# Kernel tuning notes

Hardware: AMD Instinct MI355X
Metric: run time of the kernel (lower is better)

## Reference

```python
import jax, jax.numpy as jnp
import numpy as np

DIM = 192
RC = 16
M = 64
LN_EPS = 1e-5
NORM_EPS = 1e-12


def _layernorm(x, g, b):
    mu = jnp.mean(x, axis=-1, keepdims=True)
    var = jnp.mean((x - mu) ** 2, axis=-1, keepdims=True)
    return (x - mu) / jnp.sqrt(var + LN_EPS) * g + b


def _l2norm(x):
    n = jnp.sqrt(jnp.sum(x * x, axis=-1, keepdims=True))
    return x / jnp.maximum(n, NORM_EPS)


def setup_inputs() -> dict:
    key = jax.random.key(0)
    ks = jax.random.split(key, 12)
    B, N = 8, 16384
    s_q = 1.0 / np.sqrt(DIM)
    inp = {
        "x": jax.random.normal(ks[0], (B, N, DIM), jnp.float32),
        "dict_tokens": jax.random.normal(ks[1], (B, M, DIM), jnp.float32),
        "H": 128,
        "W": 128,
        "wq_w": jax.random.normal(ks[2], (DIM, RC), jnp.float32) * s_q,
        "wq_b": jnp.zeros((RC,), jnp.float32),
        "wk_w": jax.random.normal(ks[3], (DIM, RC), jnp.float32) * s_q,
        "wk_b": jnp.zeros((RC,), jnp.float32),
        "wv_w": jax.random.normal(ks[4], (DIM, DIM), jnp.float32) * s_q,
        "wv_b": jnp.zeros((DIM,), jnp.float32),
        "qn_g": jnp.ones((RC,), jnp.float32),
        "qn_b": jnp.zeros((RC,), jnp.float32),
        "kn_g": jnp.ones((RC,), jnp.float32),
        "kn_b": jnp.zeros((RC,), jnp.float32),
        "conv_w": jax.random.normal(ks[5], (DIM, 1, 3, 3), jnp.float32) / 3.0,
        "conv_b": jnp.zeros((DIM,), jnp.float32),
        "temperature": jnp.ones((1,), jnp.float32),
    }
    return inp


def reference(x, dict_tokens, H, W, wq_w, wq_b, wk_w, wk_b, wv_w, wv_b,
              qn_g, qn_b, kn_g, kn_b, conv_w, conv_b, temperature):
    # q: (B,N,rc), k: (B,M,rc)
    q = _l2norm(_layernorm(x @ wq_w + wq_b, qn_g, qn_b))
    k = _l2norm(_layernorm(dict_tokens @ wk_w + wk_b, kn_g, kn_b))
    # cosine-similarity attention with clamped temperature
    attn = jnp.einsum("bnr,bmr->bnm", q, k) / jnp.maximum(temperature, 0.5)
    attn = jax.nn.softmax(attn, axis=-1)
    # value + depthwise-conv refinement over the M token axis (Mx1 image)
    v = dict_tokens @ wv_w + wv_b                       # (B,M,C)
    v_img = jnp.transpose(v, (0, 2, 1))[..., None]      # (B,C,M,1)
    v_img = jax.lax.conv_general_dilated(
        v_img, conv_w, window_strides=(1, 1), padding=((1, 1), (1, 1)),
        dimension_numbers=("NCHW", "OIHW", "NCHW"), feature_group_count=DIM)
    v_img = v_img + conv_b[None, :, None, None]
    v_img = jax.nn.gelu(v_img, approximate=False)
    v = jnp.transpose(v_img[..., 0], (0, 2, 1))         # (B,M,C)
    out = jnp.einsum("bnm,bmc->bnc", attn, v)           # (B,N,C)
    return out, attn
```

## Files before the change

### kernel.cpp

```cpp
#include <hip/hip_runtime.h>
#include <math.h>

#define B_   8
#define N_   16384
#define M_   64
#define C_   192
#define RC_  16

#define FMA4(acc, s, v) \
    acc.x = fmaf(s, v.x, acc.x); acc.y = fmaf(s, v.y, acc.y); \
    acc.z = fmaf(s, v.z, acc.z); acc.w = fmaf(s, v.w, acc.w)

__global__ __launch_bounds__(256) void k_prep_kernel(
    const float* __restrict__ dict,
    const float* __restrict__ wv_w, const float* __restrict__ wv_b,
    const float* __restrict__ conv_w, const float* __restrict__ conv_b,
    const float* __restrict__ wk_w, const float* __restrict__ wk_b,
    const float* __restrict__ kn_g, const float* __restrict__ kn_b,
    float* __restrict__ ws_vg, float* __restrict__ ws_k)
{
    const int b   = blockIdx.x >> 6;
    const int m   = blockIdx.x & 63;
    const int tid = threadIdx.x;
    const float* d0 = dict + (b * M_ + m) * C_;

    if (tid < 192) {
        const int c = tid;
        const bool hm = (m > 0), hp = (m < M_ - 1);
        const float* dm = hm ? d0 - C_ : d0;
        const float* dp = hp ? d0 + C_ : d0;
        float am = 0.f, ac = 0.f, ap = 0.f;
        #pragma unroll 4
        for (int d = 0; d < C_; ++d) {
            const float w = wv_w[d * C_ + c];
            am = fmaf(dm[d], w, am);
            ac = fmaf(d0[d], w, ac);
            ap = fmaf(dp[d], w, ap);
        }
        const float bia = wv_b[c];
        const float up = hm ? (am + bia) : 0.f;
        const float ct = ac + bia;
        const float dn = hp ? (ap + bia) : 0.f;
        float t = conv_b[c];
        t = fmaf(up, conv_w[c*9 + 1], t);
        t = fmaf(ct, conv_w[c*9 + 4], t);
        t = fmaf(dn, conv_w[c*9 + 7], t);
        ws_vg[(b * M_ + m) * C_ + c] = 0.5f * t * (1.0f + erff(t * 0.70710678118654752f));
    } else if (tid < 196) {
        const int j4 = tid - 192;
        const int c0 = j4 * 4;
        float a0 = wk_b[c0+0], a1 = wk_b[c0+1], a2 = wk_b[c0+2], a3 = wk_b[c0+3];
        #pragma unroll 4
        for (int d4 = 0; d4 < C_/4; ++d4) {
            const float4 xv = ((const float4*)d0)[d4];
            const float4 w0 = *(const float4*)&wk_w[(d4*4+0)*RC_ + c0];
            const float4 w1 = *(const float4*)&wk_w[(d4*4+1)*RC_ + c0];
            const float4 w2 = *(const float4*)&wk_w[(d4*4+2)*RC_ + c0];
            const float4 w3 = *(const float4*)&wk_w[(d4*4+3)*RC_ + c0];
            a0 = fmaf(xv.x, w0.x, a0); a1 = fmaf(xv.x, w0.y, a1); a2 = fmaf(xv.x, w0.z, a2); a3 = fmaf(xv.x, w0.w, a3);
            a0 = fmaf(xv.y, w1.x, a0); a1 = fmaf(xv.y, w1.y, a1); a2 = fmaf(xv.y, w1.z, a2); a3 = fmaf(xv.y, w1.w, a3);
            a0 = fmaf(xv.z, w2.x, a0); a1 = fmaf(xv.z, w2.y, a1); a2 = fmaf(xv.z, w2.z, a2); a3 = fmaf(xv.z, w2.w, a3);
            a0 = fmaf(xv.w, w3.x, a0); a1 = fmaf(xv.w, w3.y, a1); a2 = fmaf(xv.w, w3.z, a2); a3 = fmaf(xv.w, w3.w, a3);
        }
        float s  = a0 + a1 + a2 + a3;
        float ss = a0*a0 + a1*a1 + a2*a2 + a3*a3;
        s  += __shfl_xor(s, 1);  s  += __shfl_xor(s, 2);
        ss += __shfl_xor(ss, 1); ss += __shfl_xor(ss, 2);
        const float mu   = s * (1.0f/16.0f);
        const float var  = ss * (1.0f/16.0f) - mu*mu;
        const float rstd = rsqrtf(var + 1e-5f);
        const float4 g4 = *(const float4*)&kn_g[c0];
        const float4 b4 = *(const float4*)&kn_b[c0];
        const float y0 = (a0 - mu) * rstd * g4.x + b4.x;
        const float y1 = (a1 - mu) * rstd * g4.y + b4.y;
        const float y2 = (a2 - mu) * rstd * g4.z + b4.z;
        const float y3 = (a3 - mu) * rstd * g4.w + b4.w;
        float n2 = y0*y0 + y1*y1 + y2*y2 + y3*y3;
        n2 += __shfl_xor(n2, 1); n2 += __shfl_xor(n2, 2);
        const float inv = 1.0f / fmaxf(sqrtf(n2), 1e-12f);
        float4 o; o.x = y0*inv; o.y = y1*inv; o.z = y2*inv; o.w = y3*inv;
        *(float4*)&ws_k[(b * M_ + m) * RC_ + c0] = o;
    }
}

__global__ __launch_bounds__(256, 2) void k_main_kernel(
    const float* __restrict__ x, const float* __restrict__ ws_k,
    const float* __restrict__ ws_vg,
    const float* __restrict__ wq_w, const float* __restrict__ wq_b,
    const float* __restrict__ qn_g, const float* __restrict__ qn_b,
    const float* __restrict__ temp,
    float* __restrict__ out, float* __restrict__ attn_out)
{
    __shared__ float vg_s[M_ * C_];
    __shared__ float k_s[M_ * RC_];

    const int tid   = threadIdx.x;
    const int b     = blockIdx.x >> 8;
    const int n0    = (blockIdx.x & 255) * M_;
    const int lane  = tid & 63;
    const int lbase = lane & ~3;

    {
        const float4* vgb4 = (const float4*)(ws_vg + b * (M_ * C_));
        float4*       vgs4 = (float4*)vg_s;
        #pragma unroll
        for (int i = 0; i < 12; ++i)
            vgs4[tid + 256 * i] = vgb4[tid + 256 * i];
        ((float4*)k_s)[tid] = ((const float4*)(ws_k + b * (M_ * RC_)))[tid];
    }

    const int r  = tid >> 2;
    const int j4 = tid & 3;
    const int c0 = j4 * 4;

    const float* xr = x + (size_t)(b * N_ + n0 + r) * C_;
    float a0 = wq_b[c0+0], a1 = wq_b[c0+1], a2 = wq_b[c0+2], a3 = wq_b[c0+3];
    #pragma unroll 4
    for (int d4 = 0; d4 < C_/4; ++d4) {
        const float4 xv = ((const float4*)xr)[d4];
        const float4 w0 = *(const float4*)&wq_w[(d4*4+0)*RC_ + c0];
        const float4 w1 = *(const float4*)&wq_w[(d4*4+1)*RC_ + c0];
        const float4 w2 = *(const float4*)&wq_w[(d4*4+2)*RC_ + c0];
        const float4 w3 = *(const float4*)&wq_w[(d4*4+3)*RC_ + c0];
        a0 = fmaf(xv.x, w0.x, a0); a1 = fmaf(xv.x, w0.y, a1); a2 = fmaf(xv.x, w0.z, a2); a3 = fmaf(xv.x, w0.w, a3);
        a0 = fmaf(xv.y, w1.x, a0); a1 = fmaf(xv.y, w1.y, a1); a2 = fmaf(xv.y, w1.z, a2); a3 = fmaf(xv.y, w1.w, a3);
        a0 = fmaf(xv.z, w2.x, a0); a1 = fmaf(xv.z, w2.y, a1); a2 = fmaf(xv.z, w2.z, a2); a3 = fmaf(xv.z, w2.w, a3);
        a0 = fmaf(xv.w, w3.x, a0); a1 = fmaf(xv.w, w3.y, a1); a2 = fmaf(xv.w, w3.z, a2); a3 = fmaf(xv.w, w3.w, a3);
    }
    float4 q[4];
    {
        float s  = a0 + a1 + a2 + a3;
        float ss = a0*a0 + a1*a1 + a2*a2 + a3*a3;
        s  += __shfl_xor(s, 1);  s  += __shfl_xor(s, 2);
        ss += __shfl_xor(ss, 1); ss += __shfl_xor(ss, 2);
        const float mu   = s * (1.0f/16.0f);
        const float var  = ss * (1.0f/16.0f) - mu*mu;
        const float rstd = rsqrtf(var + 1e-5f);
        const float4 g4 = *(const float4*)&qn_g[c0];
        const float4 b4 = *(const float4*)&qn_b[c0];
        const float y0 = (a0 - mu) * rstd * g4.x + b4.x;
        const float y1 = (a1 - mu) * rstd * g4.y + b4.y;
        const float y2 = (a2 - mu) * rstd * g4.z + b4.z;
        const float y3 = (a3 - mu) * rstd * g4.w + b4.w;
        float n2 = y0*y0 + y1*y1 + y2*y2 + y3*y3;
        n2 += __shfl_xor(n2, 1); n2 += __shfl_xor(n2, 2);
        const float inv = 1.0f / fmaxf(sqrtf(n2), 1e-12f);
        float4 o; o.x = y0*inv; o.y = y1*inv; o.z = y2*inv; o.w = y3*inv;
        #pragma unroll
        for (int j = 0; j < 4; ++j) {
            q[j].x = __shfl(o.x, lbase + j);
            q[j].y = __shfl(o.y, lbase + j);
            q[j].z = __shfl(o.z, lbase + j);
            q[j].w = __shfl(o.w, lbase + j);
        }
    }
    const float tinv = 1.0f / fmaxf(temp[0], 0.5f);

    __syncthreads();

    float sc[16];
    {
        #pragma unroll
        for (int mm = 0; mm < 16; ++mm) {
            const int m = mm*4 + j4;
            const float4 k0 = *(const float4*)&k_s[m*RC_ + 0];
            const float4 k1 = *(const float4*)&k_s[m*RC_ + 4];
            const float4 k2 = *(const float4*)&k_s[m*RC_ + 8];
            const float4 k3 = *(const float4*)&k_s[m*RC_ + 12];
            float d = q[0].x*k0.x;
            d = fmaf(q[0].y, k0.y, d); d = fmaf(q[0].z, k0.z, d); d = fmaf(q[0].w, k0.w, d);
            d = fmaf(q[1].x, k1.x, d); d = fmaf(q[1].y, k1.y, d); d = fmaf(q[1].z, k1.z, d); d = fmaf(q[1].w, k1.w, d);
            d = fmaf(q[2].x, k2.x, d); d = fmaf(q[2].y, k2.y, d); d = fmaf(q[2].z, k2.z, d); d = fmaf(q[2].w, k2.w, d);
            d = fmaf(q[3].x, k3.x, d); d = fmaf(q[3].y, k3.y, d); d = fmaf(q[3].z, k3.z, d); d = fmaf(q[3].w, k3.w, d);
            sc[mm] = d * tinv;
        }
        float mx = sc[0];
        #pragma unroll
        for (int mm = 1; mm < 16; ++mm) mx = fmaxf(mx, sc[mm]);
        mx = fmaxf(mx, __shfl_xor(mx, 1)); mx = fmaxf(mx, __shfl_xor(mx, 2));
        float es = 0.0f;
        #pragma unroll
        for (int mm = 0; mm < 16; ++mm) { sc[mm] = expf(sc[mm] - mx); es += sc[mm]; }
        es += __shfl_xor(es, 1); es += __shfl_xor(es, 2);
        const float einv = 1.0f / es;
        float* aw = attn_out + (size_t)(b * N_ + n0 + r) * M_;
        #pragma unroll
        for (int mm = 0; mm < 16; ++mm) {
            sc[mm] *= einv;
            aw[mm*4 + j4] = sc[mm];
        }
    }

    {
        const int w0lane = tid & 63;
        const int rql = w0lane >> 4;
        const int cq  = w0lane & 15;
        const int wv  = tid >> 6;
        const int bl  = rql * 16;

        float4 ac0[3], ac1[3], ac2[3], ac3[3];
        #pragma unroll
        for (int t = 0; t < 3; ++t) {
            ac0[t] = make_float4(0.f,0.f,0.f,0.f);
            ac1[t] = make_float4(0.f,0.f,0.f,0.f);
            ac2[t] = make_float4(0.f,0.f,0.f,0.f);
            ac3[t] = make_float4(0.f,0.f,0.f,0.f);
        }
        #pragma unroll
        for (int m = 0; m < M_; ++m) {
            const float p0 = __shfl(sc[m >> 2], bl + 0  + (m & 3));
            const float p1 = __shfl(sc[m >> 2], bl + 4  + (m & 3));
            const float p2 = __shfl(sc[m >> 2], bl + 8  + (m & 3));
            const float p3 = __shfl(sc[m >> 2], bl + 12 + (m & 3));
            const float4* vr = (const float4*)(vg_s + m*C_ + cq*12);
            #pragma unroll
            for (int t = 0; t < 3; ++t) {
                const float4 v = vr[t];
                FMA4(ac0[t], p0, v);
                FMA4(ac1[t], p1, v);
                FMA4(ac2[t], p2, v);
                FMA4(ac3[t], p3, v);
            }
        }
        const int row0 = 16*wv + 4*rql;
        float* o0 = out + (size_t)(b * N_ + n0 + row0) * C_ + cq*12;
        #pragma unroll
        for (int t = 0; t < 3; ++t) {
            *(float4*)&o0[t*4]          = ac0[t];
            *(float4*)&o0[C_   + t*4]   = ac1[t];
            *(float4*)&o0[2*C_ + t*4]   = ac2[t];
            *(float4*)&o0[3*C_ + t*4]   = ac3[t];
        }
    }
}

extern "C" void kernel_launch(void* const* d_in, const int* in_sizes, int n_in,
                              void* d_out, int out_size, void* d_ws, size_t ws_size,
                              hipStream_t stream) {
    const float* x      = (const float*)d_in[0];
    const float* dict   = (const float*)d_in[1];
    const float* wq_w   = (const float*)d_in[4];
    const float* wq_b   = (const float*)d_in[5];
    const float* wk_w   = (const float*)d_in[6];
    const float* wk_b   = (const float*)d_in[7];
    const float* wv_w   = (const float*)d_in[8];
    const float* wv_b   = (const float*)d_in[9];
    const float* qn_g   = (const float*)d_in[10];
    const float* qn_b   = (const float*)d_in[11];
    const float* kn_g   = (const float*)d_in[12];
    const float* kn_b   = (const float*)d_in[13];
    const float* conv_w = (const float*)d_in[14];
    const float* conv_b = (const float*)d_in[15];
    const float* temp   = (const float*)d_in[16];

    float* out  = (float*)d_out;
    float* attn = out + (size_t)B_ * N_ * C_;

    float* ws_vg = (float*)d_ws;
    float* ws_k  = ws_vg + B_ * M_ * C_;

    k_prep_kernel<<<B_ * M_,        256, 0, stream>>>(dict, wv_w, wv_b, conv_w, conv_b,
                                                      wk_w, wk_b, kn_g, kn_b, ws_vg, ws_k);
    k_main_kernel<<<B_ * (N_ / M_), 256, 0, stream>>>(x, ws_k, ws_vg, wq_w, wq_b,
                                                      qn_g, qn_b, temp, out, attn);
}
```

Baseline: 339.0 us.

## Split fused attention kernel into separate score and output kernels

Replaces the single fused kernel with two kernels. The first computes the query projection, normalization and softmax, writing attention rows with contiguous float4 stores and reading keys directly from global memory. The second reloads the attention from global memory, transposes it through shared memory, and computes the attention-times-value product for four 64-row tiles per block, which amortizes the value-tile load. This removes shuffle-heavy broadcast and shared-memory pressure from the fused kernel, at the cost of an extra full read of the attention matrix and an additional launch.

New measurement: 392.3 us. 15.7% more time.

```diff
diff --git a/kernel.cpp b/kernel.cpp
--- a/kernel.cpp
+++ b/kernel.cpp
@@ -6,6 +6,7 @@
 #define M_   64
 #define C_   192
 #define RC_  16
+#define ATS  68
 
 #define FMA4(acc, s, v) \
     acc.x = fmaf(s, v.x, acc.x); acc.y = fmaf(s, v.y, acc.y); \
@@ -83,32 +84,17 @@
     }
 }
 
-__global__ __launch_bounds__(256, 2) void k_main_kernel(
+__global__ __launch_bounds__(256, 2) void k_q_kernel(
     const float* __restrict__ x, const float* __restrict__ ws_k,
-    const float* __restrict__ ws_vg,
     const float* __restrict__ wq_w, const float* __restrict__ wq_b,
     const float* __restrict__ qn_g, const float* __restrict__ qn_b,
-    const float* __restrict__ temp,
-    float* __restrict__ out, float* __restrict__ attn_out)
+    const float* __restrict__ temp, float* __restrict__ attn_out)
 {
-    __shared__ float vg_s[M_ * C_];
-    __shared__ float k_s[M_ * RC_];
-
     const int tid   = threadIdx.x;
     const int b     = blockIdx.x >> 8;
     const int n0    = (blockIdx.x & 255) * M_;
     const int lane  = tid & 63;
     const int lbase = lane & ~3;
-
-    {
-        const float4* vgb4 = (const float4*)(ws_vg + b * (M_ * C_));
-        float4*       vgs4 = (float4*)vg_s;
-        #pragma unroll
-        for (int i = 0; i < 12; ++i)
-            vgs4[tid + 256 * i] = vgb4[tid + 256 * i];
-        ((float4*)k_s)[tid] = ((const float4*)(ws_k + b * (M_ * RC_)))[tid];
-    }
-
     const int r  = tid >> 2;
     const int j4 = tid & 3;
     const int c0 = j4 * 4;
@@ -156,17 +142,16 @@
     }
     const float tinv = 1.0f / fmaxf(temp[0], 0.5f);
 
-    __syncthreads();
-
-    float sc[16];
     {
+        const float* kb = ws_k + b * (M_ * RC_);
+        float sc[16];
         #pragma unroll
         for (int mm = 0; mm < 16; ++mm) {
-            const int m = mm*4 + j4;
-            const float4 k0 = *(const float4*)&k_s[m*RC_ + 0];
-            const float4 k1 = *(const float4*)&k_s[m*RC_ + 4];
-            const float4 k2 = *(const float4*)&k_s[m*RC_ + 8];
-            const float4 k3 = *(const float4*)&k_s[m*RC_ + 12];
+            const int m = j4*16 + mm;
+            const float4 k0 = *(const float4*)&kb[m*RC_ + 0];
+            const float4 k1 = *(const float4*)&kb[m*RC_ + 4];
+            const float4 k2 = *(const float4*)&kb[m*RC_ + 8];
+            const float4 k3 = *(const float4*)&kb[m*RC_ + 12];
             float d = q[0].x*k0.x;
             d = fmaf(q[0].y, k0.y, d); d = fmaf(q[0].z, k0.z, d); d = fmaf(q[0].w, k0.w, d);
             d = fmaf(q[1].x, k1.x, d); d = fmaf(q[1].y, k1.y, d); d = fmaf(q[1].z, k1.z, d); d = fmaf(q[1].w, k1.w, d);
@@ -183,54 +168,88 @@
         for (int mm = 0; mm < 16; ++mm) { sc[mm] = expf(sc[mm] - mx); es += sc[mm]; }
         es += __shfl_xor(es, 1); es += __shfl_xor(es, 2);
         const float einv = 1.0f / es;
-        float* aw = attn_out + (size_t)(b * N_ + n0 + r) * M_;
-        #pragma unroll
-        for (int mm = 0; mm < 16; ++mm) {
-            sc[mm] *= einv;
-            aw[mm*4 + j4] = sc[mm];
-        }
-    }
+        float* aw = attn_out + (size_t)(b * N_ + n0 + r) * M_ + j4*16;
+        #pragma unroll
+        for (int mq = 0; mq < 4; ++mq) {
+            float4 av;
+            av.x = sc[mq*4+0]*einv; av.y = sc[mq*4+1]*einv;
+            av.z = sc[mq*4+2]*einv; av.w = sc[mq*4+3]*einv;
+            ((float4*)aw)[mq] = av;
+        }
+    }
+}
+
+__global__ __launch_bounds__(256, 2) void k_out_kernel(
+    const float* __restrict__ attn_g, const float* __restrict__ ws_vg,
+    float* __restrict__ out)
+{
+    __shared__ float vg_s[M_ * C_];
+    __shared__ float at_t[M_ * ATS];
+
+    const int tid    = threadIdx.x;
+    const int b      = blockIdx.x >> 6;
+    const int n_base = (blockIdx.x & 63) * 256;
 
     {
-        const int w0lane = tid & 63;
-        const int rql = w0lane >> 4;
-        const int cq  = w0lane & 15;
-        const int wv  = tid >> 6;
-        const int bl  = rql * 16;
+        const float4* src = (const float4*)(ws_vg + b * (M_ * C_));
+        float4*       dst = (float4*)vg_s;
+        #pragma unroll
+        for (int i = 0; i < 12; ++i)
+            dst[tid + 256 * i] = src[tid + 256 * i];
+    }
+
+    const int w0lane = tid & 63;
+    const int rql = w0lane >> 4;
+    const int cq  = w0lane & 15;
+    const int wv  = tid >> 6;
+    const int rs  = tid >> 4;
+    const int m0  = (tid & 15) * 4;
+
+    for (int t = 0; t < 4; ++t) {
+        const int n0 = n_base + t * 64;
+
+        #pragma unroll
+        for (int rr = 0; rr < 4; ++rr) {
+            const int row = rs + 16 * rr;
+            const float4 g = *(const float4*)&attn_g[(size_t)(b * N_ + n0 + row) * M_ + m0];
+            at_t[(m0+0)*ATS + row] = g.x;
+            at_t[(m0+1)*ATS + row] = g.y;
+            at_t[(m0+2)*ATS + row] = g.z;
+            at_t[(m0+3)*ATS + row] = g.w;
+        }
+        __syncthreads();
 
         float4 ac0[3], ac1[3], ac2[3], ac3[3];
         #pragma unroll
-        for (int t = 0; t < 3; ++t) {
-            ac0[t] = make_float4(0.f,0.f,0.f,0.f);
-            ac1[t] = make_float4(0.f,0.f,0.f,0.f);
-            ac2[t] = make_float4(0.f,0.f,0.f,0.f);
-            ac3[t] = make_float4(0.f,0.f,0.f,0.f);
-        }
-        #pragma unroll
+        for (int tt = 0; tt < 3; ++tt) {
+            ac0[tt] = make_float4(0.f,0.f,0.f,0.f);
+            ac1[tt] = make_float4(0.f,0.f,0.f,0.f);
+            ac2[tt] = make_float4(0.f,0.f,0.f,0.f);
+            ac3[tt] = make_float4(0.f,0.f,0.f,0.f);
+        }
+        #pragma unroll 4
         for (int m = 0; m < M_; ++m) {
-            const float p0 = __shfl(sc[m >> 2], bl + 0  + (m & 3));
-            const float p1 = __shfl(sc[m >> 2], bl + 4  + (m & 3));
-            const float p2 = __shfl(sc[m >> 2], bl + 8  + (m & 3));
-            const float p3 = __shfl(sc[m >> 2], bl + 12 + (m & 3));
+            const float4 av = *(const float4*)&at_t[m*ATS + 16*wv + 4*rql];
             const float4* vr = (const float4*)(vg_s + m*C_ + cq*12);
             #pragma unroll
-            for (int t = 0; t < 3; ++t) {
-                const float4 v = vr[t];
-                FMA4(ac0[t], p0, v);
-                FMA4(ac1[t], p1, v);
-                FMA4(ac2[t], p2, v);
-                FMA4(ac3[t], p3, v);
+            for (int tt = 0; tt < 3; ++tt) {
+                const float4 v = vr[tt];
+                FMA4(ac0[tt], av.x, v);
+                FMA4(ac1[tt], av.y, v);
+                FMA4(ac2[tt], av.z, v);
+                FMA4(ac3[tt], av.w, v);
             }
         }
         const int row0 = 16*wv + 4*rql;
         float* o0 = out + (size_t)(b * N_ + n0 + row0) * C_ + cq*12;
         #pragma unroll
-        for (int t = 0; t < 3; ++t) {
-            *(float4*)&o0[t*4]          = ac0[t];
-            *(float4*)&o0[C_   + t*4]   = ac1[t];
-            *(float4*)&o0[2*C_ + t*4]   = ac2[t];
-            *(float4*)&o0[3*C_ + t*4]   = ac3[t];
-        }
+        for (int tt = 0; tt < 3; ++tt) {
+            *(float4*)&o0[tt*4]        = ac0[tt];
+            *(float4*)&o0[C_   + tt*4] = ac1[tt];
+            *(float4*)&o0[2*C_ + tt*4] = ac2[tt];
+            *(float4*)&o0[3*C_ + tt*4] = ac3[tt];
+        }
+        __syncthreads();
     }
 }
 
@@ -261,6 +280,7 @@
 
     k_prep_kernel<<<B_ * M_,        256, 0, stream>>>(dict, wv_w, wv_b, conv_w, conv_b,
                                                       wk_w, wk_b, kn_g, kn_b, ws_vg, ws_k);
-    k_main_kernel<<<B_ * (N_ / M_), 256, 0, stream>>>(x, ws_k, ws_vg, wq_w, wq_b,
-                                                      qn_g, qn_b, temp, out, attn);
-}
+    k_q_kernel   <<<B_ * (N_ / M_), 256, 0, stream>>>(x, ws_k, wq_w, wq_b,
+                                                      qn_g, qn_b, temp, attn);
+    k_out_kernel <<<B_ * (N_ / 256), 256, 0, stream>>>(attn, ws_vg, out);
+}
```
